# Performance work log

Measured on AMD Instinct MI355X. Metric: run time of the kernel, lower is better.

## Reference

```python
import jax, jax.numpy as jnp
import numpy as np

B, S, HID, HEADS, DK, CLUE, EMB_N = 32, 256, 1024, 16, 64, 64, 200


def _rel_idx(n):
    a = jnp.arange(n)
    return jnp.abs(a[:, None] - a[None, :])  # [n, n] int


def setup_inputs() -> dict:
    key = jax.random.key(0)
    ks = jax.random.split(key, 13)
    s = 0.02
    return {
        "q": jax.random.normal(ks[0], (B, S, HID), jnp.float32),
        "k": jax.random.normal(ks[1], (B, S, HID), jnp.float32),
        "v": jax.random.normal(ks[2], (B, S, HID), jnp.float32),
        "clue_len": CLUE,
        "mask": jax.random.randint(ks[3], (B, S, 1), 0, 2, jnp.int32),
        "Wq": jax.random.normal(ks[4], (HID, HID), jnp.float32) * s,
        "bq": jnp.zeros((HID,), jnp.float32),
        "Wk": jax.random.normal(ks[5], (HID, HID), jnp.float32) * s,
        "bk": jnp.zeros((HID,), jnp.float32),
        "Wv": jax.random.normal(ks[6], (HID, HID), jnp.float32) * s,
        "bv": jnp.zeros((HID,), jnp.float32),
        "Wo": jax.random.normal(ks[7], (HID, HID), jnp.float32) * s,
        "bo": jnp.zeros((HID,), jnp.float32),
        "emb": jax.random.normal(ks[8], (EMB_N, 1), jnp.float32) * s,
    }


def reference(q, k, v, clue_len, mask, Wq, bq, Wk, bk, Wv, bv, Wo, bo, emb):
    Bx, Sx, _ = q.shape
    scale = DK ** -0.5

    # 'QA1', att_bias is None: build relative-position index matrix, lookup bias
    na = Sx - clue_len
    fp = jnp.ones((Sx, Sx), jnp.int32)
    fp = fp.at[clue_len:, clue_len:].set(_rel_idx(na))
    fp = fp.at[:clue_len, :clue_len].set(_rel_idx(clue_len))
    bias = emb[fp, 0]  # [S, S] float

    qh = (q @ Wq + bq).reshape(Bx, Sx, HEADS, DK).transpose(0, 2, 1, 3)  # bhsd
    kh = (k @ Wk + bk).reshape(Bx, Sx, HEADS, DK).transpose(0, 2, 1, 3)
    vh = (v @ Wv + bv).reshape(Bx, Sx, HEADS, DK).transpose(0, 2, 1, 3)

    # symmetric mask: mask * mask^T -> [B, 1, S, S], broadcast over heads
    m = mask[:, None, :, :].astype(jnp.float32)          # [B,1,S,1]
    m2 = m * jnp.swapaxes(m, 2, 3)                        # [B,1,S,S]
    keep = m2 > 0

    scores = jnp.einsum("bhqd,bhkd->bhqk", qh, kh) * scale + bias[None, None]
    scores = jnp.where(keep, scores, jnp.float32(-1e9))
    # masked_softmax: stable softmax on masked scores, zero out masked entries
    att = jax.nn.softmax(scores, axis=3) * keep.astype(scores.dtype)
    # dropout rate is 0.0 -> identity

    out = jnp.einsum("bhqk,bhkd->bhqd", att, vh)
    out = out.transpose(0, 2, 1, 3).reshape(Bx, Sx, HEADS * DK)
    out = out @ Wo + bo

    embedding = jnp.broadcast_to(bias[None, None], (Bx, HEADS, Sx, Sx))
    return out, embedding, att
```

## Files before the change

### kernel.cpp

```cpp
#include <hip/hip_runtime.h>
#include <stdint.h>
#include <type_traits>

typedef __bf16 bf16_t;
typedef bf16_t bf16x8 __attribute__((ext_vector_type(8)));
typedef float f32x4 __attribute__((ext_vector_type(4)));

__device__ __forceinline__ unsigned short f2bf(float f) {
  union { float f; uint32_t u; } v; v.f = f;
  uint32_t u = v.u;
  uint32_t r = (u + 0x7FFFu + ((u >> 16) & 1u)) >> 16;
  return (unsigned short)r;
}

__device__ __forceinline__ void gload16(const unsigned short* g, unsigned short* l) {
  auto gp = (const __attribute__((address_space(1))) unsigned short*)(g);
  auto lp = (__attribute__((address_space(3))) unsigned short*)(l);
  __builtin_amdgcn_global_load_lds(gp, lp, 16, 0, 0);
}

__global__ void bias_kernel(const float* __restrict__ emb,
                            const int* __restrict__ cluep,
                            float* __restrict__ bias) {
  int i = blockIdx.x, j = threadIdx.x;
  int clue = cluep[0];
  int d;
  if (i >= clue && j >= clue) d = abs(i - j);
  else if (i < clue && j < clue) d = abs(i - j);
  else d = 1;
  bias[i * 256 + j] = emb[d];
}

__global__ void emb_bcast(const float* __restrict__ bias, float* __restrict__ out) {
  const float4* b4 = reinterpret_cast<const float4*>(bias);
  float4* o4 = reinterpret_cast<float4*>(out);
  const int n4 = 33554432 / 4;
  for (int i = blockIdx.x * blockDim.x + threadIdx.x; i < n4; i += gridDim.x * blockDim.x)
    o4[i] = b4[i & 16383];
}

__global__ void cvt_bf16(const float* __restrict__ in, unsigned short* __restrict__ out) {
  const int n8 = 8388608 / 8;
  for (int i = blockIdx.x * blockDim.x + threadIdx.x; i < n8; i += gridDim.x * blockDim.x) {
    float4 a = reinterpret_cast<const float4*>(in)[2 * i];
    float4 b = reinterpret_cast<const float4*>(in)[2 * i + 1];
    ushort4 p, q;
    p.x = f2bf(a.x); p.y = f2bf(a.y); p.z = f2bf(a.z); p.w = f2bf(a.w);
    q.x = f2bf(b.x); q.y = f2bf(b.y); q.z = f2bf(b.z); q.w = f2bf(b.w);
    reinterpret_cast<ushort4*>(out)[2 * i] = p;
    reinterpret_cast<ushort4*>(out)[2 * i + 1] = q;
  }
}

__global__ __launch_bounds__(256) void wtrans(const float* __restrict__ in,
                                              unsigned short* __restrict__ out) {
  __shared__ float tile[32][33];
  const int t = threadIdx.x;
  const int tx = t & 31, ty = t >> 5;
  const int k0 = blockIdx.x * 32, n0 = blockIdx.y * 32;
  #pragma unroll
  for (int p = 0; p < 4; ++p) {
    int r = ty + p * 8;
    tile[r][tx] = in[(size_t)(k0 + r) * 1024 + n0 + tx];
  }
  __syncthreads();
  #pragma unroll
  for (int p = 0; p < 4; ++p) {
    int r = ty + p * 8;
    out[(size_t)(n0 + r) * 1024 + k0 + tx] = f2bf(tile[tx][r]);
  }
}

constexpr int GK = 1024, GN = 1024;

template<int OMODE>
__global__ __launch_bounds__(256, 2) void gemm_kernel(
    const unsigned short* __restrict__ A, const unsigned short* __restrict__ BT,
    const float* __restrict__ bvec, void* __restrict__ Cout) {
  __shared__ unsigned short Alds[128 * 64];
  __shared__ unsigned short Blds[128 * 64];
  const int t = threadIdx.x;
  const int lane = t & 63;
  const int w = t >> 6;
  const int wr = (w >> 1) * 64;
  const int wc = (w & 1) * 64;
  const int m0 = blockIdx.y * 128;
  const int n0 = blockIdx.x * 128;
  const int lg = lane >> 4;
  const int lr = lane & 15;

  const int srow = w * 32 + (lane >> 3);
  const int gch  = (lane & 7) ^ ((lane >> 3) & 7);

  f32x4 acc[4][4] = {};

  for (int k0 = 0; k0 < GK; k0 += 64) {
    #pragma unroll
    for (int i = 0; i < 4; ++i) {
      gload16(A  + (size_t)(m0 + srow + i * 8) * GK + k0 + gch * 8,
              &Alds[(w * 32 + i * 8) * 64]);
      gload16(BT + (size_t)(n0 + srow + i * 8) * GK + k0 + gch * 8,
              &Blds[(w * 32 + i * 8) * 64]);
    }
    __syncthreads();
    #pragma unroll
    for (int ks = 0; ks < 2; ++ks) {
      bf16x8 af[4], bfr[4];
      #pragma unroll
      for (int m = 0; m < 4; ++m) {
        const int r = wr + m * 16 + lr;
        const int cc = (ks * 4 + lg) ^ (lr & 7);
        af[m] = *reinterpret_cast<const bf16x8*>(&Alds[r * 64 + cc * 8]);
      }
      #pragma unroll
      for (int n = 0; n < 4; ++n) {
        const int r = wc + n * 16 + lr;
        const int cc = (ks * 4 + lg) ^ (lr & 7);
        bfr[n] = *reinterpret_cast<const bf16x8*>(&Blds[r * 64 + cc * 8]);
      }
      #pragma unroll
      for (int m = 0; m < 4; ++m) {
        #pragma unroll
        for (int n = 0; n < 4; ++n)
          acc[m][n] = __builtin_amdgcn_mfma_f32_16x16x32_bf16(af[m], bfr[n], acc[m][n], 0, 0, 0);
      }
    }
    __syncthreads();
  }

  #pragma unroll
  for (int m = 0; m < 4; ++m) {
    #pragma unroll
    for (int n = 0; n < 4; ++n) {
      const int col = n0 + wc + n * 16 + lr;
      const float bv = bvec[col];
      const int rbase = m0 + wr + m * 16 + lg * 4;
      if constexpr (OMODE == 0) {
        unsigned short* C = (unsigned short*)Cout;
        #pragma unroll
        for (int j = 0; j < 4; ++j)
          C[(size_t)(rbase + j) * GN + col] = f2bf(acc[m][n][j] + bv);
      } else if constexpr (OMODE == 1) {
        unsigned short* C = (unsigned short*)Cout;
        const int b = rbase >> 8, s = rbase & 255;
        const int h = col >> 6, d = col & 63;
        ushort4 pk;
        pk.x = f2bf(acc[m][n][0] + bv);
        pk.y = f2bf(acc[m][n][1] + bv);
        pk.z = f2bf(acc[m][n][2] + bv);
        pk.w = f2bf(acc[m][n][3] + bv);
        *reinterpret_cast<ushort4*>(&C[(size_t)((b * 16 + h) * 64 + d) * 256 + s]) = pk;
      } else {
        float* C = (float*)Cout;
        #pragma unroll
        for (int j = 0; j < 4; ++j)
          C[(size_t)(rbase + j) * GN + col] = acc[m][n][j] + bv;
      }
    }
  }
}

__device__ __forceinline__ int pidx(int row, int c) {
  return (row * 256 + c) ^ ((row & 15) << 3);
}

__global__ __launch_bounds__(256, 2) void attn_kernel(
    const unsigned short* __restrict__ qh, const unsigned short* __restrict__ kh,
    const unsigned short* __restrict__ vhT, const float* __restrict__ bias,
    const int* __restrict__ mask, float* __restrict__ att_out,
    unsigned short* __restrict__ attn_out) {
  __shared__ unsigned short P[128 * 256];
  const int t = threadIdx.x;
  const int lane = t & 63, w = t >> 6;
  const int half = blockIdx.x, h = blockIdx.y, b = blockIdx.z;
  const int rows0 = half * 128;
  const int wrow = w * 32;
  const int lg = lane >> 4, lr = lane & 15;
  const float scale = 0.125f;

  bf16x8 qf[2][2];
  #pragma unroll
  for (int m = 0; m < 2; ++m)
    #pragma unroll
    for (int ks = 0; ks < 2; ++ks)
      qf[m][ks] = *reinterpret_cast<const bf16x8*>(
          qh + (size_t)(b * 256 + rows0 + wrow + m * 16 + lr) * 1024 + h * 64 + ks * 32 + lg * 8);

  int rowm[2][4];
  #pragma unroll
  for (int m = 0; m < 2; ++m)
    #pragma unroll
    for (int j = 0; j < 4; ++j)
      rowm[m][j] = mask[b * 256 + rows0 + wrow + m * 16 + lg * 4 + j];

  float psum[2][4] = {};

  for (int ct = 0; ct < 4; ++ct) {
    f32x4 acc[2][4] = {};
    #pragma unroll
    for (int ks = 0; ks < 2; ++ks) {
      bf16x8 kf[4];
      #pragma unroll
      for (int n = 0; n < 4; ++n)
        kf[n] = *reinterpret_cast<const bf16x8*>(
            kh + (size_t)(b * 256 + ct * 64 + n * 16 + lr) * 1024 + h * 64 + ks * 32 + lg * 8);
      #pragma unroll
      for (int m = 0; m < 2; ++m)
        #pragma unroll
        for (int n = 0; n < 4; ++n)
          acc[m][n] = __builtin_amdgcn_mfma_f32_16x16x32_bf16(qf[m][ks], kf[n], acc[m][n], 0, 0, 0);
    }
    #pragma unroll
    for (int n = 0; n < 4; ++n) {
      const int c = ct * 64 + n * 16 + lr;
      const int colm = mask[b * 256 + c];
      #pragma unroll
      for (int m = 0; m < 2; ++m) {
        const int rloc = wrow + m * 16 + lg * 4;
        #pragma unroll
        for (int j = 0; j < 4; ++j) {
          float s = acc[m][n][j] * scale + bias[(rows0 + rloc + j) * 256 + c];
          float p = (rowm[m][j] & colm) ? __expf(s) : 0.f;
          psum[m][j] += p;
          P[pidx(rloc + j, c)] = f2bf(p);
        }
      }
    }
  }

  #pragma unroll
  for (int off = 1; off < 16; off <<= 1)
    #pragma unroll
    for (int m = 0; m < 2; ++m)
      #pragma unroll
      for (int j = 0; j < 4; ++j)
        psum[m][j] += __shfl_xor(psum[m][j], off);

  const size_t att_base = (size_t)(b * 16 + h) * 65536;
  #pragma unroll
  for (int it = 0; it < 16; ++it) {
    const int m2 = it >> 3;
    const int lg2 = (it >> 1) & 3;
    const int b0 = (2 * it) & 3;
    const float s0 = __shfl(psum[m2][b0], lg2 * 16);
    const float s1 = __shfl(psum[m2][b0 + 1], lg2 * 16);
    const int rloc = wrow + it * 2 + (lane >> 5);
    const int rabs = rows0 + rloc;
    const float sum = (lane >= 32) ? s1 : s0;
    const float inv = sum > 0.f ? 1.f / sum : 0.f;
    const int c8 = (lane & 31) * 8;
    bf16x8 pv = *reinterpret_cast<const bf16x8*>(&P[pidx(rloc, c8)]);
    float4 o1, o2;
    o1.x = (float)pv[0] * inv; o1.y = (float)pv[1] * inv;
    o1.z = (float)pv[2] * inv; o1.w = (float)pv[3] * inv;
    o2.x = (float)pv[4] * inv; o2.y = (float)pv[5] * inv;
    o2.z = (float)pv[6] * inv; o2.w = (float)pv[7] * inv;
    *reinterpret_cast<float4*>(&att_out[att_base + (size_t)rabs * 256 + c8]) = o1;
    *reinterpret_cast<float4*>(&att_out[att_base + (size_t)rabs * 256 + c8 + 4]) = o2;
  }

  f32x4 oacc[2][4] = {};
  for (int ks = 0; ks < 8; ++ks) {
    bf16x8 pa[2], vf[4];
    #pragma unroll
    for (int m = 0; m < 2; ++m)
      pa[m] = *reinterpret_cast<const bf16x8*>(&P[pidx(wrow + m * 16 + lr, ks * 32 + lg * 8)]);
    #pragma unroll
    for (int dn = 0; dn < 4; ++dn)
      vf[dn] = *reinterpret_cast<const bf16x8*>(
          vhT + (size_t)((b * 16 + h) * 64 + dn * 16 + lr) * 256 + ks * 32 + lg * 8);
    #pragma unroll
    for (int m = 0; m < 2; ++m)
      #pragma unroll
      for (int dn = 0; dn < 4; ++dn)
        oacc[m][dn] = __builtin_amdgcn_mfma_f32_16x16x32_bf16(pa[m], vf[dn], oacc[m][dn], 0, 0, 0);
  }
  #pragma unroll
  for (int m = 0; m < 2; ++m) {
    #pragma unroll
    for (int dn = 0; dn < 4; ++dn) {
      #pragma unroll
      for (int j = 0; j < 4; ++j) {
        const int rloc = wrow + m * 16 + lg * 4 + j;
        const float sum = psum[m][j];
        const float inv = sum > 0.f ? 1.f / sum : 0.f;
        attn_out[(size_t)(b * 256 + rows0 + rloc) * 1024 + h * 64 + dn * 16 + lr] =
            f2bf(oacc[m][dn][j] * inv);
      }
    }
  }
}

extern "C" void kernel_launch(void* const* d_in, const int* in_sizes, int n_in,
                              void* d_out, int out_size, void* d_ws, size_t ws_size,
                              hipStream_t stream) {
  (void)in_sizes; (void)n_in; (void)out_size; (void)ws_size;
  const float* q    = (const float*)d_in[0];
  const float* k    = (const float*)d_in[1];
  const float* v    = (const float*)d_in[2];
  const int*   clue = (const int*)d_in[3];
  const int*   mask = (const int*)d_in[4];
  const float* Wq   = (const float*)d_in[5];
  const float* bq   = (const float*)d_in[6];
  const float* Wk   = (const float*)d_in[7];
  const float* bk   = (const float*)d_in[8];
  const float* Wv   = (const float*)d_in[9];
  const float* bv   = (const float*)d_in[10];
  const float* Wo   = (const float*)d_in[11];
  const float* bo   = (const float*)d_in[12];
  const float* emb  = (const float*)d_in[13];

  char* ws = (char*)d_ws;
  float*          biasb = (float*)(ws);
  unsigned short* WTq   = (unsigned short*)(ws + (256u << 10));
  unsigned short* WTk   = (unsigned short*)(ws + (256u << 10) + (1u << 22));
  unsigned short* WTv   = (unsigned short*)(ws + (256u << 10) + (2u << 22));
  unsigned short* WTo   = (unsigned short*)(ws + (256u << 10) + (3u << 22));
  size_t off = (256u << 10) + (4u << 22);
  unsigned short* qh    = (unsigned short*)(ws + off); off += (16u << 20);
  unsigned short* kh    = (unsigned short*)(ws + off); off += (16u << 20);
  unsigned short* vhT   = (unsigned short*)(ws + off); off += (16u << 20);
  unsigned short* aout  = (unsigned short*)(ws + off); off += (16u << 20);
  unsigned short* qb    = (unsigned short*)(ws + off); off += (16u << 20);
  unsigned short* kb    = (unsigned short*)(ws + off); off += (16u << 20);
  unsigned short* vb    = (unsigned short*)(ws + off);

  float* out  = (float*)d_out;
  float* embo = out + 8388608;
  float* atto = out + 41943040;

  bias_kernel<<<256, 256, 0, stream>>>(emb, clue, biasb);
  emb_bcast<<<4096, 256, 0, stream>>>(biasb, embo);
  wtrans<<<dim3(32, 32), 256, 0, stream>>>(Wq, WTq);
  wtrans<<<dim3(32, 32), 256, 0, stream>>>(Wk, WTk);
  wtrans<<<dim3(32, 32), 256, 0, stream>>>(Wv, WTv);
  wtrans<<<dim3(32, 32), 256, 0, stream>>>(Wo, WTo);

  cvt_bf16<<<1024, 256, 0, stream>>>(q, qb);
  cvt_bf16<<<1024, 256, 0, stream>>>(k, kb);
  cvt_bf16<<<1024, 256, 0, stream>>>(v, vb);

  gemm_kernel<0><<<dim3(8, 64), 256, 0, stream>>>(qb, WTq, bq, qh);
  gemm_kernel<0><<<dim3(8, 64), 256, 0, stream>>>(kb, WTk, bk, kh);
  gemm_kernel<1><<<dim3(8, 64), 256, 0, stream>>>(vb, WTv, bv, vhT);

  attn_kernel<<<dim3(2, 16, 32), 256, 0, stream>>>(qh, kh, vhT, biasb, mask, atto, aout);

  gemm_kernel<2><<<dim3(8, 64), 256, 0, stream>>>(aout, WTo, bo, out);
}
```

Measured before the change: 603.6 us.

## Merge prep kernels, batch QKV GEMMs, compute bias inline, add MFMA priority

Replaces the bias, broadcast, weight-transpose and conversion kernels with a single prep kernel that dispatches work by block ID. The three QKV projection GEMMs become one launch using a z grid dimension, with occupancy raised to 3. The attention kernel now computes the relative-position bias directly from emb instead of reading a precomputed bias matrix. The float-to-bf16 conversion uses the native cast, and MFMA blocks are wrapped in s_setprio. The aim is fewer launches, fewer serialization points and less memory traffic, at the cost of a runtime mode branch in the GEMM epilogue and possible register pressure at 3 waves.

After: 572.7 us. 1.05x faster.

```diff
diff --git a/kernel.cpp b/kernel.cpp
--- a/kernel.cpp
+++ b/kernel.cpp
@@ -1,16 +1,15 @@
 #include <hip/hip_runtime.h>
 #include <stdint.h>
-#include <type_traits>
 
 typedef __bf16 bf16_t;
 typedef bf16_t bf16x8 __attribute__((ext_vector_type(8)));
 typedef float f32x4 __attribute__((ext_vector_type(4)));
 
 __device__ __forceinline__ unsigned short f2bf(float f) {
-  union { float f; uint32_t u; } v; v.f = f;
-  uint32_t u = v.u;
-  uint32_t r = (u + 0x7FFFu + ((u >> 16) & 1u)) >> 16;
-  return (unsigned short)r;
+  __bf16 h = (__bf16)f;
+  unsigned short u;
+  __builtin_memcpy(&u, &h, 2);
+  return u;
 }
 
 __device__ __forceinline__ void gload16(const unsigned short* g, unsigned short* l) {
@@ -19,64 +18,72 @@
   __builtin_amdgcn_global_load_lds(gp, lp, 16, 0, 0);
 }
 
-__global__ void bias_kernel(const float* __restrict__ emb,
-                            const int* __restrict__ cluep,
-                            float* __restrict__ bias) {
-  int i = blockIdx.x, j = threadIdx.x;
-  int clue = cluep[0];
-  int d;
-  if (i >= clue && j >= clue) d = abs(i - j);
-  else if (i < clue && j < clue) d = abs(i - j);
-  else d = 1;
-  bias[i * 256 + j] = emb[d];
-}
-
-__global__ void emb_bcast(const float* __restrict__ bias, float* __restrict__ out) {
-  const float4* b4 = reinterpret_cast<const float4*>(bias);
-  float4* o4 = reinterpret_cast<float4*>(out);
-  const int n4 = 33554432 / 4;
-  for (int i = blockIdx.x * blockDim.x + threadIdx.x; i < n4; i += gridDim.x * blockDim.x)
-    o4[i] = b4[i & 16383];
-}
-
-__global__ void cvt_bf16(const float* __restrict__ in, unsigned short* __restrict__ out) {
-  const int n8 = 8388608 / 8;
-  for (int i = blockIdx.x * blockDim.x + threadIdx.x; i < n8; i += gridDim.x * blockDim.x) {
-    float4 a = reinterpret_cast<const float4*>(in)[2 * i];
-    float4 b = reinterpret_cast<const float4*>(in)[2 * i + 1];
-    ushort4 p, q;
-    p.x = f2bf(a.x); p.y = f2bf(a.y); p.z = f2bf(a.z); p.w = f2bf(a.w);
-    q.x = f2bf(b.x); q.y = f2bf(b.y); q.z = f2bf(b.z); q.w = f2bf(b.w);
-    reinterpret_cast<ushort4*>(out)[2 * i] = p;
-    reinterpret_cast<ushort4*>(out)[2 * i + 1] = q;
-  }
-}
-
-__global__ __launch_bounds__(256) void wtrans(const float* __restrict__ in,
-                                              unsigned short* __restrict__ out) {
+__device__ __forceinline__ int relidx(int i, int j, int clue) {
+  return ((i >= clue) == (j >= clue)) ? (i > j ? i - j : j - i) : 1;
+}
+
+__global__ __launch_bounds__(256) void prep_kernel(
+    const float* __restrict__ q, const float* __restrict__ k, const float* __restrict__ v,
+    const float* __restrict__ Wq, const float* __restrict__ Wk,
+    const float* __restrict__ Wv, const float* __restrict__ Wo,
+    const float* __restrict__ emb, const int* __restrict__ cluep,
+    float* __restrict__ embo, unsigned short* __restrict__ qkvb,
+    unsigned short* __restrict__ WT) {
   __shared__ float tile[32][33];
-  const int t = threadIdx.x;
-  const int tx = t & 31, ty = t >> 5;
-  const int k0 = blockIdx.x * 32, n0 = blockIdx.y * 32;
-  #pragma unroll
-  for (int p = 0; p < 4; ++p) {
-    int r = ty + p * 8;
-    tile[r][tx] = in[(size_t)(k0 + r) * 1024 + n0 + tx];
-  }
-  __syncthreads();
-  #pragma unroll
-  for (int p = 0; p < 4; ++p) {
-    int r = ty + p * 8;
-    out[(size_t)(n0 + r) * 1024 + k0 + tx] = f2bf(tile[tx][r]);
+  const int bid = blockIdx.x, tid = threadIdx.x;
+
+  if (bid < 4096) {
+    const int clue = cluep[0];
+    float4* o4 = reinterpret_cast<float4*>(embo);
+    #pragma unroll
+    for (int it = 0; it < 8; ++it) {
+      const int i4 = bid * 2048 + it * 256 + tid;
+      const int fpos = (i4 & 16383) * 4;
+      const int i = fpos >> 8, j0 = fpos & 255;
+      float4 r;
+      r.x = emb[relidx(i, j0 + 0, clue)];
+      r.y = emb[relidx(i, j0 + 1, clue)];
+      r.z = emb[relidx(i, j0 + 2, clue)];
+      r.w = emb[relidx(i, j0 + 3, clue)];
+      o4[i4] = r;
+    }
+  } else if (bid < 7168) {
+    const int local = bid - 4096;
+    const int which = local >> 10, lb = local & 1023;
+    const float* in_ = which == 0 ? q : which == 1 ? k : v;
+    unsigned short* out_ = qkvb + (size_t)which * 8388608;
+    for (int i = lb * 256 + tid; i < 1048576; i += 262144) {
+      float4 a = reinterpret_cast<const float4*>(in_)[2 * i];
+      float4 b = reinterpret_cast<const float4*>(in_)[2 * i + 1];
+      ushort4 p, qq;
+      p.x = f2bf(a.x); p.y = f2bf(a.y); p.z = f2bf(a.z); p.w = f2bf(a.w);
+      qq.x = f2bf(b.x); qq.y = f2bf(b.y); qq.z = f2bf(b.z); qq.w = f2bf(b.w);
+      reinterpret_cast<ushort4*>(out_)[2 * i] = p;
+      reinterpret_cast<ushort4*>(out_)[2 * i + 1] = qq;
+    }
+  } else {
+    const int local = bid - 7168;
+    const int which = local >> 10, wl = local & 1023;
+    const float* in_ = which == 0 ? Wq : which == 1 ? Wk : which == 2 ? Wv : Wo;
+    unsigned short* out_ = WT + (size_t)which * 2097152;
+    const int tx = tid & 31, ty = tid >> 5;
+    const int k0 = (wl & 31) * 32, n0 = (wl >> 5) * 32;
+    #pragma unroll
+    for (int p = 0; p < 4; ++p)
+      tile[ty + p * 8][tx] = in_[(size_t)(k0 + ty + p * 8) * 1024 + n0 + tx];
+    __syncthreads();
+    #pragma unroll
+    for (int p = 0; p < 4; ++p)
+      out_[(size_t)(n0 + ty + p * 8) * 1024 + k0 + tx] = f2bf(tile[tx][ty + p * 8]);
   }
 }
 
 constexpr int GK = 1024, GN = 1024;
 
-template<int OMODE>
-__global__ __launch_bounds__(256, 2) void gemm_kernel(
-    const unsigned short* __restrict__ A, const unsigned short* __restrict__ BT,
-    const float* __restrict__ bvec, void* __restrict__ Cout) {
+__global__ __launch_bounds__(256, 3) void gemm_fused(
+    const unsigned short* __restrict__ Abase, const unsigned short* __restrict__ BTbase,
+    const float* __restrict__ b0, const float* __restrict__ b1, const float* __restrict__ b2,
+    void* __restrict__ Cbase, int mode) {
   __shared__ unsigned short Alds[128 * 64];
   __shared__ unsigned short Blds[128 * 64];
   const int t = threadIdx.x;
@@ -86,8 +93,13 @@
   const int wc = (w & 1) * 64;
   const int m0 = blockIdx.y * 128;
   const int n0 = blockIdx.x * 128;
+  const int zz = blockIdx.z;
   const int lg = lane >> 4;
   const int lr = lane & 15;
+
+  const unsigned short* A  = Abase + (size_t)zz * 8388608;
+  const unsigned short* BT = BTbase + (size_t)zz * 2097152;
+  const float* bvec = zz == 0 ? b0 : zz == 1 ? b1 : b2;
 
   const int srow = w * 32 + (lane >> 3);
   const int gch  = (lane & 7) ^ ((lane >> 3) & 7);
@@ -118,16 +130,19 @@
         const int cc = (ks * 4 + lg) ^ (lr & 7);
         bfr[n] = *reinterpret_cast<const bf16x8*>(&Blds[r * 64 + cc * 8]);
       }
+      __builtin_amdgcn_s_setprio(1);
       #pragma unroll
       for (int m = 0; m < 4; ++m) {
         #pragma unroll
         for (int n = 0; n < 4; ++n)
           acc[m][n] = __builtin_amdgcn_mfma_f32_16x16x32_bf16(af[m], bfr[n], acc[m][n], 0, 0, 0);
       }
+      __builtin_amdgcn_s_setprio(0);
     }
     __syncthreads();
   }
 
+  const int omode = (mode == 2) ? 2 : (zz == 2 ? 1 : 0);
   #pragma unroll
   for (int m = 0; m < 4; ++m) {
     #pragma unroll
@@ -135,13 +150,13 @@
       const int col = n0 + wc + n * 16 + lr;
       const float bv = bvec[col];
       const int rbase = m0 + wr + m * 16 + lg * 4;
-      if constexpr (OMODE == 0) {
-        unsigned short* C = (unsigned short*)Cout;
+      if (omode == 0) {
+        unsigned short* C = (unsigned short*)Cbase + (size_t)zz * 8388608;
         #pragma unroll
         for (int j = 0; j < 4; ++j)
           C[(size_t)(rbase + j) * GN + col] = f2bf(acc[m][n][j] + bv);
-      } else if constexpr (OMODE == 1) {
-        unsigned short* C = (unsigned short*)Cout;
+      } else if (omode == 1) {
+        unsigned short* C = (unsigned short*)Cbase + (size_t)zz * 8388608;
         const int b = rbase >> 8, s = rbase & 255;
         const int h = col >> 6, d = col & 63;
         ushort4 pk;
@@ -151,7 +166,7 @@
         pk.w = f2bf(acc[m][n][3] + bv);
         *reinterpret_cast<ushort4*>(&C[(size_t)((b * 16 + h) * 64 + d) * 256 + s]) = pk;
       } else {
-        float* C = (float*)Cout;
+        float* C = (float*)Cbase;
         #pragma unroll
         for (int j = 0; j < 4; ++j)
           C[(size_t)(rbase + j) * GN + col] = acc[m][n][j] + bv;
@@ -166,9 +181,9 @@
 
 __global__ __launch_bounds__(256, 2) void attn_kernel(
     const unsigned short* __restrict__ qh, const unsigned short* __restrict__ kh,
-    const unsigned short* __restrict__ vhT, const float* __restrict__ bias,
-    const int* __restrict__ mask, float* __restrict__ att_out,
-    unsigned short* __restrict__ attn_out) {
+    const unsigned short* __restrict__ vhT, const float* __restrict__ emb,
+    const int* __restrict__ cluep, const int* __restrict__ mask,
+    float* __restrict__ att_out, unsigned short* __restrict__ attn_out) {
   __shared__ unsigned short P[128 * 256];
   const int t = threadIdx.x;
   const int lane = t & 63, w = t >> 6;
@@ -177,6 +192,7 @@
   const int wrow = w * 32;
   const int lg = lane >> 4, lr = lane & 15;
   const float scale = 0.125f;
+  const int clue = cluep[0];
 
   bf16x8 qf[2][2];
   #pragma unroll
@@ -204,22 +220,27 @@
       for (int n = 0; n < 4; ++n)
         kf[n] = *reinterpret_cast<const bf16x8*>(
             kh + (size_t)(b * 256 + ct * 64 + n * 16 + lr) * 1024 + h * 64 + ks * 32 + lg * 8);
+      __builtin_amdgcn_s_setprio(1);
       #pragma unroll
       for (int m = 0; m < 2; ++m)
         #pragma unroll
         for (int n = 0; n < 4; ++n)
           acc[m][n] = __builtin_amdgcn_mfma_f32_16x16x32_bf16(qf[m][ks], kf[n], acc[m][n], 0, 0, 0);
+      __builtin_amdgcn_s_setprio(0);
     }
     #pragma unroll
     for (int n = 0; n < 4; ++n) {
       const int c = ct * 64 + n * 16 + lr;
       const int colm = mask[b * 256 + c];
+      const bool cside = c >= clue;
       #pragma unroll
       for (int m = 0; m < 2; ++m) {
         const int rloc = wrow + m * 16 + lg * 4;
         #pragma unroll
         for (int j = 0; j < 4; ++j) {
-          float s = acc[m][n][j] * scale + bias[(rows0 + rloc + j) * 256 + c];
+          const int i = rows0 + rloc + j;
+          const int d = (((i >= clue)) == cside) ? (i > c ? i - c : c - i) : 1;
+          float s = acc[m][n][j] * scale + emb[d];
           float p = (rowm[m][j] & colm) ? __expf(s) : 0.f;
           psum[m][j] += p;
           P[pidx(rloc + j, c)] = f2bf(p);
@@ -269,11 +290,13 @@
     for (int dn = 0; dn < 4; ++dn)
       vf[dn] = *reinterpret_cast<const bf16x8*>(
           vhT + (size_t)((b * 16 + h) * 64 + dn * 16 + lr) * 256 + ks * 32 + lg * 8);
+    __builtin_amdgcn_s_setprio(1);
     #pragma unroll
     for (int m = 0; m < 2; ++m)
       #pragma unroll
       for (int dn = 0; dn < 4; ++dn)
         oacc[m][dn] = __builtin_amdgcn_mfma_f32_16x16x32_bf16(pa[m], vf[dn], oacc[m][dn], 0, 0, 0);
+    __builtin_amdgcn_s_setprio(0);
   }
   #pragma unroll
   for (int m = 0; m < 2; ++m) {
@@ -311,40 +334,22 @@
   const float* emb  = (const float*)d_in[13];
 
   char* ws = (char*)d_ws;
-  float*          biasb = (float*)(ws);
-  unsigned short* WTq   = (unsigned short*)(ws + (256u << 10));
-  unsigned short* WTk   = (unsigned short*)(ws + (256u << 10) + (1u << 22));
-  unsigned short* WTv   = (unsigned short*)(ws + (256u << 10) + (2u << 22));
-  unsigned short* WTo   = (unsigned short*)(ws + (256u << 10) + (3u << 22));
-  size_t off = (256u << 10) + (4u << 22);
-  unsigned short* qh    = (unsigned short*)(ws + off); off += (16u << 20);
-  unsigned short* kh    = (unsigned short*)(ws + off); off += (16u << 20);
-  unsigned short* vhT   = (unsigned short*)(ws + off); off += (16u << 20);
-  unsigned short* aout  = (unsigned short*)(ws + off); off += (16u << 20);
-  unsigned short* qb    = (unsigned short*)(ws + off); off += (16u << 20);
-  unsigned short* kb    = (unsigned short*)(ws + off); off += (16u << 20);
-  unsigned short* vb    = (unsigned short*)(ws + off);
+  unsigned short* WT   = (unsigned short*)(ws);
+  size_t off = 16u << 20;
+  unsigned short* qh   = (unsigned short*)(ws + off); off += (16u << 20);
+  unsigned short* kh   = (unsigned short*)(ws + off); off += (16u << 20);
+  unsigned short* vhT  = (unsigned short*)(ws + off); off += (16u << 20);
+  unsigned short* aout = (unsigned short*)(ws + off); off += (16u << 20);
+  unsigned short* qkvb = (unsigned short*)(ws + off);
+  (void)kh; (void)vhT;
 
   float* out  = (float*)d_out;
   float* embo = out + 8388608;
   float* atto = out + 41943040;
 
-  bias_kernel<<<256, 256, 0, stream>>>(emb, clue, biasb);
-  emb_bcast<<<4096, 256, 0, stream>>>(biasb, embo);
-  wtrans<<<dim3(32, 32), 256, 0, stream>>>(Wq, WTq);
-  wtrans<<<dim3(32, 32), 256, 0, stream>>>(Wk, WTk);
-  wtrans<<<dim3(32, 32), 256, 0, stream>>>(Wv, WTv);
-  wtrans<<<dim3(32, 32), 256, 0, stream>>>(Wo, WTo);
-
-  cvt_bf16<<<1024, 256, 0, stream>>>(q, qb);
-  cvt_bf16<<<1024, 256, 0, stream>>>(k, kb);
-  cvt_bf16<<<1024, 256, 0, stream>>>(v, vb);
-
-  gemm_kernel<0><<<dim3(8, 64), 256, 0, stream>>>(qb, WTq, bq, qh);
-  gemm_kernel<0><<<dim3(8, 64), 256, 0, stream>>>(kb, WTk, bk, kh);
-  gemm_kernel<1><<<dim3(8, 64), 256, 0, stream>>>(vb, WTv, bv, vhT);
-
-  attn_kernel<<<dim3(2, 16, 32), 256, 0, stream>>>(qh, kh, vhT, biasb, mask, atto, aout);
-
-  gemm_kernel<2><<<dim3(8, 64), 256, 0, stream>>>(aout, WTo, bo, out);
-}
+  prep_kernel<<<11264, 256, 0, stream>>>(q, k, v, Wq, Wk, Wv, Wo, emb, clue,
+                                         embo, qkvb, WT);
+  gemm_fused<<<dim3(8, 64, 3), 256, 0, stream>>>(qkvb, WT, bq, bk, bv, qh, 0);
+  attn_kernel<<<dim3(2, 16, 32), 256, 0, stream>>>(qh, kh, vhT, emb, clue, mask, atto, aout);
+  gemm_fused<<<dim3(8, 64, 1), 256, 0, stream>>>(aout, WT + 3 * 2097152, bo, bo, bo, out, 2);
+}
```
